# Optimization experiments

Hardware: AMD Instinct MI355X
Metric: run time of the kernel (lower is better)

The kernel has to match this reference:

```python
import jax, jax.numpy as jnp
import numpy as np

HIDDEN = 1024
HORIZON = 24
BATCH, SEQ, D_IN = 256, 512, 64


def setup_inputs() -> dict:
    key = jax.random.key(0)
    k1, k2, k3, k4, k5 = jax.random.split(key, 5)
    fan_in = D_IN + HIDDEN
    # flax Dense default: lecun_normal kernel, zero bias; use scaled normal
    W = jax.random.normal(k1, (fan_in, 4 * HIDDEN), jnp.float32) / np.sqrt(fan_in)
    b = jnp.zeros((4 * HIDDEN,), jnp.float32)
    Wout = jax.random.normal(k2, (HIDDEN, HORIZON), jnp.float32) / np.sqrt(HIDDEN)
    bout = jnp.zeros((HORIZON,), jnp.float32)
    x = jax.random.normal(k3, (BATCH, SEQ, D_IN), jnp.float32)
    return {"x": x, "W": W, "b": b, "Wout": Wout, "bout": bout}


def reference(x, W, b, Wout, bout):
    B, T, D = x.shape
    H = W.shape[1] // 4

    def step(carry, x_t):
        h, c = carry
        gates = jnp.concatenate([x_t, h], axis=-1) @ W + b  # [B, 4H]
        i, f, g, o = jnp.split(gates, 4, axis=-1)
        i = jax.nn.sigmoid(i)
        f = jax.nn.sigmoid(f)
        o = jax.nn.sigmoid(o)
        g = jnp.tanh(g)
        c = f * c + i * g
        h = o * jnp.tanh(c)
        return (h, c), None

    init = (jnp.zeros((B, H), x.dtype), jnp.zeros((B, H), x.dtype))
    (h_final, _), _ = jax.lax.scan(step, init, jnp.swapaxes(x, 0, 1))
    return h_final @ Wout + bout  # [B, horizon]
```

## Files before the change

kernel.cpp:

```cpp
#include <hip/hip_runtime.h>
#include <hip/hip_fp16.h>


#define T_STEPS 512
#define HID 1024
#define GRID 256
#define NTHR 512

typedef __attribute__((ext_vector_type(8))) _Float16 half8;
typedef __attribute__((ext_vector_type(4))) float f32x4;
typedef __attribute__((ext_vector_type(2))) float f32x2;

__device__ __forceinline__ float sigm(float v) { return 1.0f / (1.0f + __expf(-v)); }
__device__ __forceinline__ float tanh_fast(float v) { return 2.0f / (1.0f + __expf(-2.0f * v)) - 1.0f; }

__global__ void pack_w(const float* __restrict__ W, _Float16* __restrict__ Wp) {
    int idx = blockIdx.x * 256 + threadIdx.x;
    const int total = 64 * 136 * 64;
    if (idx >= total) return;
    int col = idx & 63;
    int kb = (idx >> 6) % 136;
    int n = (idx >> 6) / 136;
    int oc = ((col & 3) << 10) + (n << 4) + (col >> 2);
    const float* src = W + (size_t)(kb * 8) * 4096 + oc;
    _Float16* dst = Wp + (size_t)idx * 8;
#pragma unroll
    for (int j = 0; j < 8; j++) dst[j] = (_Float16)src[(size_t)j * 4096];
}

__global__ void __launch_bounds__(NTHR, 2) lstm_persist(
    const float* __restrict__ x,
    const _Float16* __restrict__ Wp,
    const float* __restrict__ bias,
    _Float16* __restrict__ hbuf,
    float* __restrict__ hfinal,
    unsigned int* bar)
{
    __shared__ float P[4 * 64 * 64];

    int wg = blockIdx.x;
    int xcd = wg & 7, slot = wg >> 3;
    int n = (xcd << 3) + (slot & 7);
    int m = slot >> 3;
    int B0 = m << 6;

    int tid = threadIdx.x;
    int wave = tid >> 6;
    int lane = tid & 63;
    int l15 = lane & 15, l4 = lane >> 4;
    int bb = tid & 63;
    int u0 = tid >> 6;

    float breg[2][4];
#pragma unroll
    for (int q = 0; q < 2; q++) {
        int u = (u0 << 1) + q;
#pragma unroll
        for (int g = 0; g < 4; g++) breg[q][g] = bias[(g << 10) + (n << 4) + u];
    }

    float cst[2] = {0.f, 0.f};

    const size_t HB = (size_t)128 * 256 * 8;
    const _Float16* WpBase = Wp + (size_t)n * 136 * 64 * 8;

    int hc[4];
#pragma unroll
    for (int j = 0; j < 4; j++) hc[j] = (wave < 2) ? (wave + 8 * (j + 1)) : (wave + 8 * j);
    half8 wfr[4][4];
#pragma unroll
    for (int j = 0; j < 4; j++) {
        int kb = (hc[j] << 2) + l4;
        const _Float16* wp = WpBase + ((size_t)kb << 9);
#pragma unroll
        for (int nn = 0; nn < 4; nn++) wfr[j][nn] = *(const half8*)(wp + (((nn << 4) + l15) << 3));
    }

    f32x4 acc[4][4];
#pragma unroll
    for (int i = 0; i < 4; i++)
#pragma unroll
        for (int j = 0; j < 4; j++) acc[i][j] = (f32x4){0.f, 0.f, 0.f, 0.f};

    auto XPREP = [&](int tt) {
        if (wave < 2) {
            int kb = (wave << 2) + l4;
            half8 bx[4];
            const _Float16* wp = WpBase + ((size_t)kb << 9);
#pragma unroll
            for (int nn = 0; nn < 4; nn++) bx[nn] = *(const half8*)(wp + (((nn << 4) + l15) << 3));
#pragma unroll
            for (int mm = 0; mm < 4; mm++) {
                const float* xp = x + ((size_t)(B0 + (mm << 4) + l15) * T_STEPS + tt) * 64 + (kb << 3);
                f32x4 lo = *(const f32x4*)xp;
                f32x4 hi = *(const f32x4*)(xp + 4);
                half8 v;
                v[0] = (_Float16)lo[0]; v[1] = (_Float16)lo[1];
                v[2] = (_Float16)lo[2]; v[3] = (_Float16)lo[3];
                v[4] = (_Float16)hi[0]; v[5] = (_Float16)hi[1];
                v[6] = (_Float16)hi[2]; v[7] = (_Float16)hi[3];
#pragma unroll
                for (int nn = 0; nn < 4; nn++)
                    acc[mm][nn] = __builtin_amdgcn_mfma_f32_16x16x32_f16(v, bx[nn], acc[mm][nn], 0, 0, 0);
            }
        }
    };

    XPREP(0);

    for (int t = 0; t < T_STEPS; t++) {
        const _Float16* cur = hbuf + (size_t)(t & 1) * HB;
        _Float16* nxt = hbuf + (size_t)((t + 1) & 1) * HB;

        half8 ah[4][4];
#pragma unroll
        for (int j = 0; j < 4; j++) {
            int kb = (hc[j] << 2) + l4;
            unsigned long long* hp =
                (unsigned long long*)(cur + (((size_t)(kb - 8) << 8) + B0 + l15) * 8);
#pragma unroll
            for (int mm = 0; mm < 4; mm++) {
                union { unsigned long long u[2]; half8 h; } cv;
                cv.u[0] = __hip_atomic_load(hp + (mm << 5), __ATOMIC_RELAXED, __HIP_MEMORY_SCOPE_AGENT);
                cv.u[1] = __hip_atomic_load(hp + (mm << 5) + 1, __ATOMIC_RELAXED, __HIP_MEMORY_SCOPE_AGENT);
                ah[j][mm] = cv.h;
            }
        }
#pragma unroll
        for (int j = 0; j < 4; j++)
#pragma unroll
            for (int mm = 0; mm < 4; mm++)
#pragma unroll
                for (int nn = 0; nn < 4; nn++)
                    acc[mm][nn] = __builtin_amdgcn_mfma_f32_16x16x32_f16(ah[j][mm], wfr[j][nn],
                                                                         acc[mm][nn], 0, 0, 0);

        if (wave < 4) {
#pragma unroll
            for (int mm = 0; mm < 4; mm++)
#pragma unroll
                for (int nn = 0; nn < 4; nn++) {
                    int c = (nn << 4) + l15;
                    int bblk = (mm << 2) + l4;
                    int word = (((wave << 6) + c) << 6) + (((bblk ^ l15) & 15) << 2);
                    *(f32x4*)&P[word] = acc[mm][nn];
                }
        }
        __syncthreads();
        if (wave >= 4) {
            int pw = wave - 4;
#pragma unroll
            for (int mm = 0; mm < 4; mm++)
#pragma unroll
                for (int nn = 0; nn < 4; nn++) {
                    int c = (nn << 4) + l15;
                    int bblk = (mm << 2) + l4;
                    int word = (((pw << 6) + c) << 6) + (((bblk ^ l15) & 15) << 2);
                    f32x4 v = *(f32x4*)&P[word];
                    v += acc[mm][nn];
                    *(f32x4*)&P[word] = v;
                }
        }
        __syncthreads();

        union { _Float16 h2[2]; unsigned int u; } hs;
        float hvf[2];
#pragma unroll
        for (int q = 0; q < 2; q++) {
            int u = (u0 << 1) + q;
            float g4[4];
#pragma unroll
            for (int g = 0; g < 4; g++) {
                int c = (u << 2) + g;
                int word = (c << 6) + (((((bb >> 2) ^ c) & 15) << 2) | (bb & 3));
                float s = breg[q][g];
#pragma unroll
                for (int w = 0; w < 4; w++) s += P[(w << 12) + word];
                g4[g] = s;
            }
            float ig = sigm(g4[0]);
            float fg = sigm(g4[1]);
            float gg = tanh_fast(g4[2]);
            float og = sigm(g4[3]);
            float cv = fg * cst[q] + ig * gg;
            cst[q] = cv;
            float hv = og * tanh_fast(cv);
            hs.h2[q] = (_Float16)hv;
            hvf[q] = hv;
        }
        int ug0 = (n << 4) + (u0 << 1);
        {
            unsigned int* dst =
                (unsigned int*)(nxt + ((size_t)(ug0 >> 3) * 256 + B0 + bb) * 8 + (ug0 & 7));
            __hip_atomic_store(dst, hs.u, __ATOMIC_RELAXED, __HIP_MEMORY_SCOPE_AGENT);
        }
        if (t == T_STEPS - 1) {
            f32x2 hv2; hv2[0] = hvf[0]; hv2[1] = hvf[1];
            *(f32x2*)&hfinal[(size_t)(B0 + bb) * HID + ug0] = hv2;
            break;
        }

        asm volatile("s_waitcnt vmcnt(0)" ::: "memory");
        __syncthreads();
        if (tid == 0)
            __hip_atomic_store(bar + (wg << 4), (unsigned int)(t + 1), __ATOMIC_RELAXED,
                               __HIP_MEMORY_SCOPE_AGENT);
#pragma unroll
        for (int i = 0; i < 4; i++)
#pragma unroll
            for (int j = 0; j < 4; j++) acc[i][j] = (f32x4){0.f, 0.f, 0.f, 0.f};
        XPREP(t + 1);
        if (tid >= 256) {
            const unsigned int* ap = bar + ((tid - 256) << 4);
            while (__hip_atomic_load(ap, __ATOMIC_RELAXED, __HIP_MEMORY_SCOPE_AGENT) <
                   (unsigned int)(t + 1)) {
                __builtin_amdgcn_s_sleep(1);
            }
        }
        __syncthreads();
    }
}

__global__ void proj_kernel(const float* __restrict__ hfinal, const float* __restrict__ Wout,
                            const float* __restrict__ bout, float* __restrict__ out) {
    int b = blockIdx.x;
    int l = threadIdx.x;
    float acc[24];
#pragma unroll
    for (int j = 0; j < 24; j++) acc[j] = 0.f;
    for (int i = 0; i < 16; i++) {
        int k = i * 64 + l;
        float h = hfinal[(size_t)b * HID + k];
        const float* wr = Wout + (size_t)k * 24;
#pragma unroll
        for (int j = 0; j < 24; j++) acc[j] += h * wr[j];
    }
    __shared__ float red[24][65];
#pragma unroll
    for (int j = 0; j < 24; j++) red[j][l] = acc[j];
    __syncthreads();
    if (l < 24) {
        float s = bout[l];
#pragma unroll
        for (int i = 0; i < 64; i++) s += red[l][i];
        out[b * 24 + l] = s;
    }
}

extern "C" void kernel_launch(void* const* d_in, const int* in_sizes, int n_in,
                              void* d_out, int out_size, void* d_ws, size_t ws_size,
                              hipStream_t stream) {
    const float* x = (const float*)d_in[0];
    const float* W = (const float*)d_in[1];
    const float* b = (const float*)d_in[2];
    const float* Wout = (const float*)d_in[3];
    const float* bout = (const float*)d_in[4];
    float* out = (float*)d_out;

    char* ws = (char*)d_ws;
    _Float16* Wp = (_Float16*)ws;
    _Float16* hbuf = (_Float16*)(ws + 8912896);
    float* hfinal = (float*)(ws + 8912896 + 1048576);
    unsigned int* bar = (unsigned int*)(ws + 8912896 + 2097152);

    hipMemsetAsync(hbuf, 0, (size_t)128 * 256 * 8 * sizeof(_Float16), stream);
    hipMemsetAsync(bar, 0, 16384, stream);

    pack_w<<<(64 * 136 * 64 + 255) / 256, 256, 0, stream>>>(W, Wp);

    void* args[6];
    args[0] = (void*)&x;
    args[1] = (void*)&Wp;
    args[2] = (void*)&b;
    args[3] = (void*)&hbuf;
    args[4] = (void*)&hfinal;
    args[5] = (void*)&bar;
    hipLaunchCooperativeKernel((void*)lstm_persist, dim3(GRID), dim3(NTHR), args, 0, stream);

    proj_kernel<<<256, 64, 0, stream>>>(hfinal, Wout, bout, out);
}
```

Before: 3.689 ms.

## Stage h output through LDS for coalesced stores, interleave h loads with MFMA

```diff
diff --git a/kernel.cpp b/kernel.cpp
--- a/kernel.cpp
+++ b/kernel.cpp
@@ -11,8 +11,12 @@
 typedef __attribute__((ext_vector_type(4))) float f32x4;
 typedef __attribute__((ext_vector_type(2))) float f32x2;
 
-__device__ __forceinline__ float sigm(float v) { return 1.0f / (1.0f + __expf(-v)); }
-__device__ __forceinline__ float tanh_fast(float v) { return 2.0f / (1.0f + __expf(-2.0f * v)) - 1.0f; }
+__device__ __forceinline__ float sigm(float v) {
+    return __builtin_amdgcn_rcpf(1.0f + __expf(-v));
+}
+__device__ __forceinline__ float tanh_fast(float v) {
+    return 2.0f * __builtin_amdgcn_rcpf(1.0f + __expf(-2.0f * v)) - 1.0f;
+}
 
 __global__ void pack_w(const float* __restrict__ W, _Float16* __restrict__ Wp) {
     int idx = blockIdx.x * 256 + threadIdx.x;
@@ -37,6 +41,7 @@
     unsigned int* bar)
 {
     __shared__ float P[4 * 64 * 64];
+    _Float16* hstage = (_Float16*)P;
 
     int wg = blockIdx.x;
     int xcd = wg & 7, slot = wg >> 3;
@@ -64,13 +69,10 @@
     const size_t HB = (size_t)128 * 256 * 8;
     const _Float16* WpBase = Wp + (size_t)n * 136 * 64 * 8;
 
-    int hc[4];
-#pragma unroll
-    for (int j = 0; j < 4; j++) hc[j] = (wave < 2) ? (wave + 8 * (j + 1)) : (wave + 8 * j);
     half8 wfr[4][4];
 #pragma unroll
     for (int j = 0; j < 4; j++) {
-        int kb = (hc[j] << 2) + l4;
+        int kb = ((2 + wave + 8 * j) << 2) + l4;
         const _Float16* wp = WpBase + ((size_t)kb << 9);
 #pragma unroll
         for (int nn = 0; nn < 4; nn++) wfr[j][nn] = *(const half8*)(wp + (((nn << 4) + l15) << 3));
@@ -83,8 +85,8 @@
         for (int j = 0; j < 4; j++) acc[i][j] = (f32x4){0.f, 0.f, 0.f, 0.f};
 
     auto XPREP = [&](int tt) {
-        if (wave < 2) {
-            int kb = (wave << 2) + l4;
+        if (wave == 2 || wave == 3) {
+            int kb = ((wave - 2) << 2) + l4;
             half8 bx[4];
             const _Float16* wp = WpBase + ((size_t)kb << 9);
 #pragma unroll
@@ -112,28 +114,26 @@
         const _Float16* cur = hbuf + (size_t)(t & 1) * HB;
         _Float16* nxt = hbuf + (size_t)((t + 1) & 1) * HB;
 
-        half8 ah[4][4];
 #pragma unroll
         for (int j = 0; j < 4; j++) {
-            int kb = (hc[j] << 2) + l4;
+            int kb = ((2 + wave + 8 * j) << 2) + l4;
             unsigned long long* hp =
                 (unsigned long long*)(cur + (((size_t)(kb - 8) << 8) + B0 + l15) * 8);
+            half8 ah[4];
 #pragma unroll
             for (int mm = 0; mm < 4; mm++) {
                 union { unsigned long long u[2]; half8 h; } cv;
                 cv.u[0] = __hip_atomic_load(hp + (mm << 5), __ATOMIC_RELAXED, __HIP_MEMORY_SCOPE_AGENT);
                 cv.u[1] = __hip_atomic_load(hp + (mm << 5) + 1, __ATOMIC_RELAXED, __HIP_MEMORY_SCOPE_AGENT);
-                ah[j][mm] = cv.h;
-            }
-        }
-#pragma unroll
-        for (int j = 0; j < 4; j++)
+                ah[mm] = cv.h;
+            }
 #pragma unroll
             for (int mm = 0; mm < 4; mm++)
 #pragma unroll
                 for (int nn = 0; nn < 4; nn++)
-                    acc[mm][nn] = __builtin_amdgcn_mfma_f32_16x16x32_f16(ah[j][mm], wfr[j][nn],
+                    acc[mm][nn] = __builtin_amdgcn_mfma_f32_16x16x32_f16(ah[mm], wfr[j][nn],
                                                                          acc[mm][nn], 0, 0, 0);
+        }
 
         if (wave < 4) {
 #pragma unroll
@@ -188,20 +188,28 @@
             hs.h2[q] = (_Float16)hv;
             hvf[q] = hv;
         }
-        int ug0 = (n << 4) + (u0 << 1);
-        {
-            unsigned int* dst =
-                (unsigned int*)(nxt + ((size_t)(ug0 >> 3) * 256 + B0 + bb) * 8 + (ug0 & 7));
-            __hip_atomic_store(dst, hs.u, __ATOMIC_RELAXED, __HIP_MEMORY_SCOPE_AGENT);
-        }
         if (t == T_STEPS - 1) {
+            int ug0 = (n << 4) + (u0 << 1);
             f32x2 hv2; hv2[0] = hvf[0]; hv2[1] = hvf[1];
             *(f32x2*)&hfinal[(size_t)(B0 + bb) * HID + ug0] = hv2;
             break;
         }
 
+        __syncthreads();
+        *(unsigned int*)&hstage[(bb << 4) + (u0 << 1)] = hs.u;
+        __syncthreads();
+        if (tid < 128) {
+            int row = tid >> 1, hf = tid & 1;
+            union { half8 h; unsigned long long u[2]; } v;
+            v.h = *(const half8*)&hstage[(row << 4) + (hf << 3)];
+            unsigned long long* dst =
+                (unsigned long long*)(nxt + (((size_t)((n << 1) + hf) << 8) + B0 + row) * 8);
+            __hip_atomic_store(dst, v.u[0], __ATOMIC_RELAXED, __HIP_MEMORY_SCOPE_AGENT);
+            __hip_atomic_store(dst + 1, v.u[1], __ATOMIC_RELAXED, __HIP_MEMORY_SCOPE_AGENT);
+        }
         asm volatile("s_waitcnt vmcnt(0)" ::: "memory");
         __syncthreads();
+
         if (tid == 0)
             __hip_atomic_store(bar + (wg << 4), (unsigned int)(t + 1), __ATOMIC_RELAXED,
                                __HIP_MEMORY_SCOPE_AGENT);
```

New measurement: 3.561 ms. -3.5%, faster.
